# Kernel tuning notes

Measured on AMD Instinct MI355X. Metric: run time of the kernel, lower is better.

Reference implementation:

```python
import jax, jax.numpy as jnp
import numpy as np

B, T, C, WD = 8, 2048, 768, 512
TD, CD = 384, 3072   # tokens_dim=0.5*C, channels_dim=4*C
H1 = C               # default hidden of token StyleGLUs
EPS = 1e-6


def _ln(x, g, b):
    mu = jnp.mean(x, -1, keepdims=True)
    v = jnp.mean((x - mu) ** 2, -1, keepdims=True)
    return (x - mu) * jax.lax.rsqrt(v + EPS) * g + b


def _style_glu(x, w, gW, gb, sW, sb, mW, mb):
    # gate linear -> GLU -> style-modulated matmul (modulation folded into einsum)
    h = x @ gW + gb                       # [B,T,H]
    a, gt = jnp.split(h, 2, axis=-1)
    a = a * jax.nn.sigmoid(gt)            # [B,T,H/2]
    s = w @ sW + sb                       # [B,H/2] per-sample style scale
    return jnp.einsum('bth,bh,ho->bto', a, s, mW) + mb


def setup_inputs() -> dict:
    key = jax.random.key(0)
    ks = iter(jax.random.split(key, 40))
    def nrm(*s, sc=0.02):
        return jax.random.normal(next(ks), s, dtype=jnp.float32) * sc
    return dict(
        x=jax.random.normal(next(ks), (B, T, C), dtype=jnp.float32),
        w=jax.random.normal(next(ks), (B, 2, WD), dtype=jnp.float32),
        ln1_g=jnp.ones(C, jnp.float32), ln1_b=jnp.zeros(C, jnp.float32),
        ln2_g=jnp.ones(C, jnp.float32), ln2_b=jnp.zeros(C, jnp.float32),
        g1_W=nrm(C, H1), g1_b=jnp.zeros(H1, jnp.float32),
        s1_W=nrm(WD, H1 // 2), s1_b=jnp.zeros(H1 // 2, jnp.float32),
        m1_W=nrm(H1 // 2, TD, sc=0.05), m1_b=nrm(TD, sc=0.05),
        g2_W=nrm(C, H1), g2_b=jnp.zeros(H1, jnp.float32),
        s2_W=nrm(WD, H1 // 2), s2_b=jnp.zeros(H1 // 2, jnp.float32),
        m2_W=nrm(H1 // 2, TD, sc=0.05), m2_b=nrm(TD, sc=0.05),
        gs_W=nrm(C, CD), gs_b=jnp.zeros(CD, jnp.float32),
        ss_W=nrm(WD, CD // 2), ss_b=jnp.zeros(CD // 2, jnp.float32),
        ms_W=nrm(CD // 2, C, sc=0.05), ms_b=nrm(C, sc=0.05),
        r1_W=nrm(C, C), r1_b=jnp.zeros(C, jnp.float32),
        r2_W=nrm(C // 2, C), r2_b=jnp.zeros(C, jnp.float32),
    )


def reference(x, w, ln1_g, ln1_b, ln2_g, ln2_b,
              g1_W, g1_b, s1_W, s1_b, m1_W, m1_b,
              g2_W, g2_b, s2_W, s2_b, m2_W, m2_b,
              gs_W, gs_b, ss_W, ss_b, ms_W, ms_b,
              r1_W, r1_b, r2_W, r2_b):
    x = _ln(x, ln1_g, ln1_b)
    w0, w1 = w[:, 0], w[:, 1]
    # --- StyleHyperMixer token mixing (eval: dropout/droppath = identity) ---
    h1 = _style_glu(x, w0, g1_W, g1_b, s1_W, s1_b, m1_W, m1_b)  # [B,T,TD]
    h2 = _style_glu(x, w0, g2_W, g2_b, s2_W, s2_b, m2_W, m2_b)  # [B,T,TD]
    mix = jax.nn.gelu(jnp.einsum('btd,btc->bdc', h1, x), approximate=False)  # [B,TD,C]
    x = x + jnp.einsum('btd,bdc->btc', h2, mix)
    # --- style-modulated channel MLP ---
    x = x + _style_glu(_ln(x, ln2_g, ln2_b), w1, gs_W, gs_b, ss_W, ss_b, ms_W, ms_b)
    # --- GLU reduce ---
    h = x @ r1_W + r1_b
    a, gt = jnp.split(h, 2, axis=-1)
    return (a * jax.nn.sigmoid(gt)) @ r2_W + r2_b
```

## Files before the change

kernel.cpp:

```cpp
#include <hip/hip_runtime.h>
#include <hip/hip_bf16.h>
#include <math.h>

#define NB 8
#define NT 2048
#define NC 768
#define ROWS (NB*NT)

typedef __attribute__((ext_vector_type(8))) short s8v;
typedef __attribute__((ext_vector_type(4))) float f4v;

__device__ __forceinline__ unsigned short f2b(float f) {
    unsigned u = __builtin_bit_cast(unsigned, f);
    return (unsigned short)((u + 0x7FFFu + ((u >> 16) & 1u)) >> 16);
}

__device__ __forceinline__ void gll16(const ushort* g, ushort* l) {
    __builtin_amdgcn_global_load_lds(
        (const __attribute__((address_space(1))) void*)g,
        (__attribute__((address_space(3))) void*)l, 16, 0, 0);
}

template<int R>
__device__ __forceinline__ void stageL(ushort* __restrict__ L, const ushort* __restrict__ G,
                                       int ld, int r0, int k0, int lane, int w) {
    int rs = lane >> 2, c = lane & 3;
#pragma unroll
    for (int i = 0; i < R / 64; i++) {
        int ii = w + 4 * i;
        int row = ii * 16 + rs;
        int kc = (c ^ ((row >> 1) & 3)) << 3;
        gll16(G + (long)(r0 + row) * ld + k0 + kc, L + ii * 512);
    }
}

template<int R>
__device__ __forceinline__ void stage_f32(ushort* __restrict__ L, const float* __restrict__ G,
                                          int ld, int r0, int k0, int t) {
#pragma unroll
    for (int i = 0; i < R / 32; i++) {
        int e = i * 256 + t;
        int row = e >> 3, kc = (e & 7) * 4;
        float4 v = *(const float4*)(G + (long)(r0 + row) * ld + k0 + kc);
        ushort4 o;
        o.x = f2b(v.x); o.y = f2b(v.y); o.z = f2b(v.z); o.w = f2b(v.w);
        int c = (kc >> 3) ^ ((row >> 1) & 3);
        *(ushort4*)&L[row * 32 + c * 8 + (kc & 7)] = o;
    }
}

template<int TN, int EPI, bool HASBIAS, bool SPLITK>
__global__ __launch_bounds__(256) void gemm_mfma(
    const ushort* __restrict__ A, const ushort* __restrict__ Bt,
    float* __restrict__ Cf, ushort* __restrict__ Cb,
    int M, int N, int K, int lda, int ldb, int ldc,
    long sA, long sB, long sC, const float* __restrict__ bias)
{
    constexpr int WM = (TN == 128) ? 64 : 32;
    constexpr int TI = WM / 16;
    int zz = blockIdx.z;
    int z  = SPLITK ? (zz >> 2) : zz;
    int kb = SPLITK ? (zz & 3) * (K >> 2) : 0;
    int ke = SPLITK ? kb + (K >> 2) : K;
    const ushort* Az = A + (long)z * sA;
    const ushort* Bz = Bt + (long)z * sB;
    float*  Cfz = Cf ? Cf + (long)z * sC : nullptr;
    ushort* Cbz = Cb ? Cb + (long)z * sC : nullptr;

    int m0 = blockIdx.y * 128, n0 = blockIdx.x * TN;
    __shared__ alignas(16) ushort Al[4096];
    __shared__ alignas(16) ushort Bl[TN * 32];
    int t = threadIdx.x;
    int lane = t & 63, w = t >> 6;
    int wm = (TN == 128) ? (w >> 1) * 64 : w * 32;
    int wn = (TN == 128) ? (w & 1) * 64 : 0;
    int fr = lane & 15, q = lane >> 4;

    f4v acc[TI][4];
#pragma unroll
    for (int i = 0; i < TI; i++)
#pragma unroll
        for (int j = 0; j < 4; j++) acc[i][j] = (f4v)(0.0f);

    for (int k0 = kb; k0 < ke; k0 += 32) {
        stageL<128>(Al, Az, lda, m0, k0, lane, w);
        stageL<TN>(Bl, Bz, ldb, n0, k0, lane, w);
        __syncthreads();
        s8v af[TI], bf[4];
#pragma unroll
        for (int ti = 0; ti < TI; ti++) {
            int r = wm + ti * 16 + fr;
            af[ti] = *(const s8v*)&Al[r * 32 + ((q ^ ((r >> 1) & 3)) << 3)];
        }
#pragma unroll
        for (int tj = 0; tj < 4; tj++) {
            int r = wn + tj * 16 + fr;
            bf[tj] = *(const s8v*)&Bl[r * 32 + ((q ^ ((r >> 1) & 3)) << 3)];
        }
#pragma unroll
        for (int ti = 0; ti < TI; ti++)
#pragma unroll
            for (int tj = 0; tj < 4; tj++)
                acc[ti][tj] = __builtin_amdgcn_mfma_f32_16x16x32_bf16(
                    af[ti], bf[tj], acc[ti][tj], 0, 0, 0);
        __syncthreads();
    }

    int cr0 = q * 4;
#pragma unroll
    for (int ti = 0; ti < TI; ti++) {
#pragma unroll
        for (int tj = 0; tj < 4; tj++) {
            int n = n0 + wn + tj * 16 + fr;
            float bv = HASBIAS ? bias[n] : 0.0f;
#pragma unroll
            for (int r = 0; r < 4; r++) {
                int m = m0 + wm + ti * 16 + cr0 + r;
                long idx = (long)m * ldc + n;
                float v = acc[ti][tj][r] + bv;
                if (EPI == 0) {
                    Cbz[idx] = f2b(v);
                } else if (EPI == 5) {
                    Cfz[idx] = v;
                } else if (EPI == 6) {
                    __hip_atomic_fetch_add(&Cfz[idx], v, __ATOMIC_RELAXED,
                                           __HIP_MEMORY_SCOPE_AGENT);
                } else {
                    v += Cfz[idx];
                    if (EPI == 3) Cfz[idx] = v;
                    if (EPI == 4) Cbz[idx] = f2b(v);
                }
            }
        }
    }
}

template<int TN, bool HAS_S, bool AF32>
__global__ __launch_bounds__(256) void gemm_glu_mfma(
    const void* __restrict__ A,
    const ushort* __restrict__ Bt0, const ushort* __restrict__ Bt1,
    ushort* __restrict__ C0, ushort* __restrict__ C1,
    int M, int Nh, int K, int lda,
    const float* __restrict__ bias0, const float* __restrict__ bias1,
    const float* __restrict__ s0, const float* __restrict__ s1, int bofs)
{
    constexpr int WM = (TN == 128) ? 64 : 32;
    constexpr int TI = WM / 16;
    int z = blockIdx.z;
    const ushort* Bt = z ? Bt1 : Bt0;
    ushort* Cb = z ? C1 : C0;
    const float* bias = z ? bias1 : bias0;
    const float* s = z ? s1 : s0;

    int m0 = blockIdx.y * 128, n0 = blockIdx.x * TN;
    __shared__ alignas(16) ushort Al[4096];
    __shared__ alignas(16) ushort B1[TN * 32];
    __shared__ alignas(16) ushort B2[TN * 32];
    int t = threadIdx.x;
    int lane = t & 63, w = t >> 6;
    int wm = (TN == 128) ? (w >> 1) * 64 : w * 32;
    int wn = (TN == 128) ? (w & 1) * 64 : 0;
    int fr = lane & 15, q = lane >> 4;

    f4v acc1[TI][4], acc2[TI][4];
#pragma unroll
    for (int i = 0; i < TI; i++)
#pragma unroll
        for (int j = 0; j < 4; j++) { acc1[i][j] = (f4v)(0.0f); acc2[i][j] = (f4v)(0.0f); }

    for (int k0 = 0; k0 < K; k0 += 32) {
        stageL<TN>(B1, Bt, K, n0, k0, lane, w);
        stageL<TN>(B2, Bt, K, Nh + n0, k0, lane, w);
        if (AF32) stage_f32<128>(Al, (const float*)A, lda, m0, k0, t);
        else      stageL<128>(Al, (const ushort*)A, lda, m0, k0, lane, w);
        __syncthreads();
        s8v af[TI], b1f[4], b2f[4];
#pragma unroll
        for (int ti = 0; ti < TI; ti++) {
            int r = wm + ti * 16 + fr;
            af[ti] = *(const s8v*)&Al[r * 32 + ((q ^ ((r >> 1) & 3)) << 3)];
        }
#pragma unroll
        for (int tj = 0; tj < 4; tj++) {
            int r = wn + tj * 16 + fr;
            int o = r * 32 + ((q ^ ((r >> 1) & 3)) << 3);
            b1f[tj] = *(const s8v*)&B1[o];
            b2f[tj] = *(const s8v*)&B2[o];
        }
#pragma unroll
        for (int ti = 0; ti < TI; ti++)
#pragma unroll
            for (int tj = 0; tj < 4; tj++) {
                acc1[ti][tj] = __builtin_amdgcn_mfma_f32_16x16x32_bf16(af[ti], b1f[tj], acc1[ti][tj], 0, 0, 0);
                acc2[ti][tj] = __builtin_amdgcn_mfma_f32_16x16x32_bf16(af[ti], b2f[tj], acc2[ti][tj], 0, 0, 0);
            }
        __syncthreads();
    }

    int cr0 = q * 4;
#pragma unroll
    for (int ti = 0; ti < TI; ti++) {
        int bb = ((m0 + wm + ti * 16 + cr0) >> 11) + bofs;
#pragma unroll
        for (int tj = 0; tj < 4; tj++) {
            int n = n0 + wn + tj * 16 + fr;
            float bv = bias[n], bg = bias[Nh + n];
            float sv = HAS_S ? s[(long)bb * Nh + n] : 1.0f;
#pragma unroll
            for (int r = 0; r < 4; r++) {
                int m = m0 + wm + ti * 16 + cr0 + r;
                float vv = acc1[ti][tj][r] + bv;
                float gg = acc2[ti][tj][r] + bg;
                float a = vv * (1.0f / (1.0f + expf(-gg)));
                if (HAS_S) a *= sv;
                Cb[(long)m * Nh + n] = f2b(a);
            }
        }
    }
}

__global__ __launch_bounds__(256) void gelu_cast_kernel(const float* __restrict__ in,
                                                        ushort* __restrict__ out) {
    int i4 = (blockIdx.x * 256 + threadIdx.x) * 4;
    float4 v = *(const float4*)(in + i4);
    ushort4 o;
    o.x = f2b(0.5f * v.x * (1.0f + erff(v.x * 0.70710678118654752440f)));
    o.y = f2b(0.5f * v.y * (1.0f + erff(v.y * 0.70710678118654752440f)));
    o.z = f2b(0.5f * v.z * (1.0f + erff(v.z * 0.70710678118654752440f)));
    o.w = f2b(0.5f * v.w * (1.0f + erff(v.w * 0.70710678118654752440f)));
    *(ushort4*)(out + i4) = o;
}

template<bool SRC_F32>
__global__ __launch_bounds__(256) void transpose_kernel(const void* __restrict__ src,
                                                        ushort* __restrict__ dst,
                                                        int R, int C, long sS, long sD) {
    int z = blockIdx.z;
    const void* S = SRC_F32 ? (const void*)((const float*)src + (long)z * sS)
                            : (const void*)((const ushort*)src + (long)z * sS);
    ushort* D = dst + (long)z * sD;
    int r0 = blockIdx.y * 64, c0 = blockIdx.x * 64;
    __shared__ ushort T[64][68];
    int t = threadIdx.x;
#pragma unroll
    for (int p = 0; p < 4; p++) {
        int e = p * 256 + t;
        int row = e >> 4, cc = (e & 15) * 4;
        ushort4 v;
        if (SRC_F32) {
            float4 f = *(const float4*)((const float*)S + (long)(r0 + row) * C + c0 + cc);
            v.x = f2b(f.x); v.y = f2b(f.y); v.z = f2b(f.z); v.w = f2b(f.w);
        } else {
            v = *(const ushort4*)((const ushort*)S + (long)(r0 + row) * C + c0 + cc);
        }
        *(ushort4*)&T[row][cc] = v;
    }
    __syncthreads();
#pragma unroll
    for (int p = 0; p < 4; p++) {
        int e = p * 256 + t;
        int crow = e >> 4, rr = (e & 15) * 4;
        ushort4 o;
        o.x = T[rr + 0][crow]; o.y = T[rr + 1][crow];
        o.z = T[rr + 2][crow]; o.w = T[rr + 3][crow];
        *(ushort4*)&D[(long)(c0 + crow) * R + r0 + rr] = o;
    }
}

__global__ __launch_bounds__(256) void castT_kernel(const float* __restrict__ W,
                                                    ushort* __restrict__ Wt, int K, int N) {
    int k = blockIdx.x * 64 + (threadIdx.x & 63);
    int n = blockIdx.y * 4 + (threadIdx.x >> 6);
    Wt[(long)n * K + k] = f2b(W[(long)k * N + n]);
}

template<bool BF16OUT>
__global__ __launch_bounds__(256) void ln_kernel(const float* __restrict__ x,
                                                 const float* __restrict__ g,
                                                 const float* __restrict__ b,
                                                 void* __restrict__ outv) {
    int row = blockIdx.x;
    const float* xr = x + (long)row * NC;
    int t = threadIdx.x;
    float v0 = xr[t], v1 = xr[t + 256], v2 = xr[t + 512];
    float s = v0 + v1 + v2;
    float s2 = v0 * v0 + v1 * v1 + v2 * v2;
    for (int off = 32; off > 0; off >>= 1) {
        s  += __shfl_down(s, off, 64);
        s2 += __shfl_down(s2, off, 64);
    }
    __shared__ float ls[4], ls2[4];
    int wid = t >> 6, lane = t & 63;
    if (lane == 0) { ls[wid] = s; ls2[wid] = s2; }
    __syncthreads();
    if (t == 0) {
        float ts = ls[0] + ls[1] + ls[2] + ls[3];
        float ts2 = ls2[0] + ls2[1] + ls2[2] + ls2[3];
        float mu = ts * (1.0f / NC);
        float var = ts2 * (1.0f / NC) - mu * mu;
        ls[0] = mu;
        ls2[0] = 1.0f / sqrtf(var + 1e-6f);
    }
    __syncthreads();
    float mu = ls[0], r = ls2[0];
#pragma unroll
    for (int i = 0; i < 3; i++) {
        int c = t + i * 256;
        float vv = (i == 0 ? v0 : (i == 1 ? v1 : v2));
        float o = (vv - mu) * r * g[c] + b[c];
        if (BF16OUT) ((ushort*)outv)[(long)row * NC + c] = f2b(o);
        else         ((float*)outv)[(long)row * NC + c] = o;
    }
}

__global__ __launch_bounds__(256) void svec_kernel(const float* __restrict__ w,
                                                   const float* __restrict__ s1W, const float* __restrict__ s1b,
                                                   const float* __restrict__ s2W, const float* __restrict__ s2b,
                                                   const float* __restrict__ ssW, const float* __restrict__ ssb,
                                                   float* __restrict__ sout) {
    int gid = blockIdx.x * 256 + threadIdx.x;
    int bb = gid / 2304;
    int r  = gid % 2304;
    const float* w0 = w + (long)bb * 1024;
    const float* w1 = w0 + 512;
    float acc = 0.f;
    if (r < 384) {
        for (int k = 0; k < 512; k++) acc += w0[k] * s1W[k * 384 + r];
        sout[bb * 384 + r] = acc + s1b[r];
    } else if (r < 768) {
        int c = r - 384;
        for (int k = 0; k < 512; k++) acc += w0[k] * s2W[k * 384 + c];
        sout[3072 + bb * 384 + c] = acc + s2b[c];
    } else {
        int c = r - 768;
        for (int k = 0; k < 512; k++) acc += w1[k] * ssW[k * 1536 + c];
        sout[6144 + bb * 1536 + c] = acc + ssb[c];
    }
}

extern "C" void kernel_launch(void* const* d_in, const int* in_sizes, int n_in,
                              void* d_out, int out_size, void* d_ws, size_t ws_size,
                              hipStream_t stream) {
    const float* x     = (const float*)d_in[0];
    const float* w     = (const float*)d_in[1];
    const float* ln1_g = (const float*)d_in[2];
    const float* ln1_b = (const float*)d_in[3];
    const float* ln2_g = (const float*)d_in[4];
    const float* ln2_b = (const float*)d_in[5];
    const float* g1_W  = (const float*)d_in[6];
    const float* g1_b  = (const float*)d_in[7];
    const float* s1_W  = (const float*)d_in[8];
    const float* s1_b  = (const float*)d_in[9];
    const float* m1_W  = (const float*)d_in[10];
    const float* m1_b  = (const float*)d_in[11];
    const float* g2_W  = (const float*)d_in[12];
    const float* g2_b  = (const float*)d_in[13];
    const float* s2_W  = (const float*)d_in[14];
    const float* s2_b  = (const float*)d_in[15];
    const float* m2_W  = (const float*)d_in[16];
    const float* m2_b  = (const float*)d_in[17];
    const float* gs_W  = (const float*)d_in[18];
    const float* gs_b  = (const float*)d_in[19];
    const float* ss_W  = (const float*)d_in[20];
    const float* ss_b  = (const float*)d_in[21];
    const float* ms_W  = (const float*)d_in[22];
    const float* ms_b  = (const float*)d_in[23];
    const float* r1_W  = (const float*)d_in[24];
    const float* r1_b  = (const float*)d_in[25];
    const float* r2_W  = (const float*)d_in[26];
    const float* r2_b  = (const float*)d_in[27];
    float* out = (float*)d_out;
    char* ws = (char*)d_ws;
    char* ob = (char*)d_out;

    float*  XLN = (float*)ws;
    ushort* A1b = (ushort*)(ws + 50331648);
    ushort* g1t = (ushort*)(ws + 62914560);
    ushort* g2t = g1t + 589824;
    ushort* m1t = g2t + 589824;
    ushort* m2t = m1t + 147456;
    ushort* gst = m2t + 147456;
    ushort* mst = gst + 2359296;
    ushort* r1t = mst + 1179648;
    ushort* r2t = r1t + 589824;
    float*  SV  = (float*)(ws + 74711040);
    ushort* H1T = A1b;
    ushort* ASq = A1b;
    ushort* ARq = A1b;

    ushort* XLNT  = (ushort*)(ob + 25165824);
    ushort* A2q   = (ushort*)(ob + 12582912);
    ushort* H2q   = (ushort*)ob;
    ushort* H1q   = (ushort*)(ob + 12582912);
    float*  MIXTf = (float*)(ob + 12582912);
    ushort* MIXTb = (ushort*)(ob + 25165824);
    ushort* X2LNq = (ushort*)(ob + 25165824);
    ushort* X3q   = (ushort*)ob;

    castT_kernel<<<dim3(12, 192), 256, 0, stream>>>(g1_W, g1t, 768, 768);
    castT_kernel<<<dim3(12, 192), 256, 0, stream>>>(g2_W, g2t, 768, 768);
    castT_kernel<<<dim3(6,  96),  256, 0, stream>>>(m1_W, m1t, 384, 384);
    castT_kernel<<<dim3(6,  96),  256, 0, stream>>>(m2_W, m2t, 384, 384);
    castT_kernel<<<dim3(12, 768), 256, 0, stream>>>(gs_W, gst, 768, 3072);
    castT_kernel<<<dim3(24, 192), 256, 0, stream>>>(ms_W, mst, 1536, 768);
    castT_kernel<<<dim3(12, 192), 256, 0, stream>>>(r1_W, r1t, 768, 768);
    castT_kernel<<<dim3(6,  192), 256, 0, stream>>>(r2_W, r2t, 384, 768);
    svec_kernel<<<72, 256, 0, stream>>>(w, s1_W, s1_b, s2_W, s2_b, ss_W, ss_b, SV);
    ln_kernel<false><<<ROWS, 256, 0, stream>>>(x, ln1_g, ln1_b, XLN);
    transpose_kernel<true><<<dim3(12, 32, NB), 256, 0, stream>>>(
        XLN, XLNT, 2048, 768, (long)2048 * 768, (long)768 * 2048);

    gemm_glu_mfma<128, true, true><<<dim3(3, 128, 2), 256, 0, stream>>>(
        XLN, g1t, g2t, A1b, A2q, ROWS, 384, 768, 768, g1_b, g2_b, SV, SV + 3072, 0);
    gemm_mfma<64, 0, true, false><<<dim3(6, 128), 256, 0, stream>>>(
        A2q, m2t, nullptr, H2q, ROWS, 384, 384, 384, 384, 384, 0, 0, 0, m2_b);
    gemm_mfma<64, 0, true, false><<<dim3(6, 128), 256, 0, stream>>>(
        A1b, m1t, nullptr, H1q, ROWS, 384, 384, 384, 384, 384, 0, 0, 0, m1_b);
    transpose_kernel<false><<<dim3(6, 32, NB), 256, 0, stream>>>(
        H1q, H1T, 2048, 384, (long)2048 * 384, (long)384 * 2048);
    hipMemsetAsync(MIXTf, 0, (size_t)NB * 768 * 384 * 4, stream);
    gemm_mfma<128, 6, false, true><<<dim3(3, 6, NB * 4), 256, 0, stream>>>(
        XLNT, H1T, MIXTf, nullptr, 768, 384, 2048, 2048, 2048, 384,
        (long)768 * 2048, (long)384 * 2048, (long)768 * 384, nullptr);
    gelu_cast_kernel<<<2304, 256, 0, stream>>>(MIXTf, MIXTb);
    gemm_mfma<128, 3, false, false><<<dim3(6, 16, NB), 256, 0, stream>>>(
        H2q, MIXTb, XLN, nullptr, 2048, 768, 384, 384, 384, 768,
        (long)2048 * 384, (long)768 * 384, (long)2048 * 768, nullptr);
    ln_kernel<true><<<ROWS, 256, 0, stream>>>(XLN, ln2_g, ln2_b, X2LNq);
    for (int ch = 0; ch < 4; ch++) {
        ushort* X2c = X2LNq + (long)ch * 4096 * 768;
        float*  XLNc = XLN + (long)ch * 4096 * 768;
        ushort* X3c = X3q + (long)ch * 4096 * 768;
        gemm_glu_mfma<64, true, false><<<dim3(24, 32), 256, 0, stream>>>(
            X2c, gst, gst, ASq, ASq, 4096, 1536, 768, 768, gs_b, gs_b,
            SV + 6144, SV + 6144, ch * 2);
        gemm_mfma<64, 4, true, false><<<dim3(12, 32), 256, 0, stream>>>(
            ASq, mst, XLNc, X3c, 4096, 768, 1536, 1536, 1536, 768, 0, 0, 0, ms_b);
    }
    gemm_glu_mfma<64, false, false><<<dim3(6, 128), 256, 0, stream>>>(
        X3q, r1t, r1t, ARq, ARq, ROWS, 384, 768, 768, r1_b, r1_b, nullptr, nullptr, 0);
    gemm_mfma<128, 5, true, false><<<dim3(6, 128), 256, 0, stream>>>(
        ARq, r2t, out, nullptr, ROWS, 768, 384, 384, 384, 768, 0, 0, 0, r2_b);
}
```

Before: 859.1 us.

## Merge weight-cast launches into one prep kernel and emit bf16 from first LN

Eight weight cast/transpose launches and the style-vector kernel are merged into a single prep kernel, which cuts launch overhead. The first layernorm now writes both fp32 and bf16 outputs, so the first GLU GEMM can stage its A tiles with direct global-to-LDS loads instead of converting fp32 per k-step. The sigmoid switches to the fast __expf, and the transpose launch is reordered after the GLU GEMM. In exchange the LN pass writes an extra bf16 copy, and __expf gives slightly lower precision.

Result: faster. 822.0 us (-4.3%).

```diff
diff --git a/kernel.cpp b/kernel.cpp
--- a/kernel.cpp
+++ b/kernel.cpp
@@ -31,21 +31,6 @@
         int row = ii * 16 + rs;
         int kc = (c ^ ((row >> 1) & 3)) << 3;
         gll16(G + (long)(r0 + row) * ld + k0 + kc, L + ii * 512);
-    }
-}
-
-template<int R>
-__device__ __forceinline__ void stage_f32(ushort* __restrict__ L, const float* __restrict__ G,
-                                          int ld, int r0, int k0, int t) {
-#pragma unroll
-    for (int i = 0; i < R / 32; i++) {
-        int e = i * 256 + t;
-        int row = e >> 3, kc = (e & 7) * 4;
-        float4 v = *(const float4*)(G + (long)(r0 + row) * ld + k0 + kc);
-        ushort4 o;
-        o.x = f2b(v.x); o.y = f2b(v.y); o.z = f2b(v.z); o.w = f2b(v.w);
-        int c = (kc >> 3) ^ ((row >> 1) & 3);
-        *(ushort4*)&L[row * 32 + c * 8 + (kc & 7)] = o;
     }
 }
 
@@ -135,9 +120,9 @@
     }
 }
 
-template<int TN, bool HAS_S, bool AF32>
+template<int TN, bool HAS_S>
 __global__ __launch_bounds__(256) void gemm_glu_mfma(
-    const void* __restrict__ A,
+    const ushort* __restrict__ A,
     const ushort* __restrict__ Bt0, const ushort* __restrict__ Bt1,
     ushort* __restrict__ C0, ushort* __restrict__ C1,
     int M, int Nh, int K, int lda,
@@ -171,8 +156,7 @@
     for (int k0 = 0; k0 < K; k0 += 32) {
         stageL<TN>(B1, Bt, K, n0, k0, lane, w);
         stageL<TN>(B2, Bt, K, Nh + n0, k0, lane, w);
-        if (AF32) stage_f32<128>(Al, (const float*)A, lda, m0, k0, t);
-        else      stageL<128>(Al, (const ushort*)A, lda, m0, k0, lane, w);
+        stageL<128>(Al, A, lda, m0, k0, lane, w);
         __syncthreads();
         s8v af[TI], b1f[4], b2f[4];
 #pragma unroll
@@ -211,7 +195,7 @@
                 int m = m0 + wm + ti * 16 + cr0 + r;
                 float vv = acc1[ti][tj][r] + bv;
                 float gg = acc2[ti][tj][r] + bg;
-                float a = vv * (1.0f / (1.0f + expf(-gg)));
+                float a = vv * (1.0f / (1.0f + __expf(-gg)));
                 if (HAS_S) a *= sv;
                 Cb[(long)m * Nh + n] = f2b(a);
             }
@@ -267,18 +251,64 @@
     }
 }
 
-__global__ __launch_bounds__(256) void castT_kernel(const float* __restrict__ W,
-                                                    ushort* __restrict__ Wt, int K, int N) {
-    int k = blockIdx.x * 64 + (threadIdx.x & 63);
-    int n = blockIdx.y * 4 + (threadIdx.x >> 6);
-    Wt[(long)n * K + k] = f2b(W[(long)k * N + n]);
-}
-
-template<bool BF16OUT>
+__global__ __launch_bounds__(256) void prep_kernel(
+    const float* __restrict__ g1_W, ushort* __restrict__ g1t,
+    const float* __restrict__ g2_W, ushort* __restrict__ g2t,
+    const float* __restrict__ m1_W, ushort* __restrict__ m1t,
+    const float* __restrict__ m2_W, ushort* __restrict__ m2t,
+    const float* __restrict__ gs_W, ushort* __restrict__ gst,
+    const float* __restrict__ ms_W, ushort* __restrict__ mst,
+    const float* __restrict__ r1_W, ushort* __restrict__ r1t,
+    const float* __restrict__ r2_W, ushort* __restrict__ r2t,
+    const float* __restrict__ w,
+    const float* __restrict__ s1W, const float* __restrict__ s1b,
+    const float* __restrict__ s2W, const float* __restrict__ s2b,
+    const float* __restrict__ ssW, const float* __restrict__ ssb,
+    float* __restrict__ sout)
+{
+    int b = blockIdx.x, t = threadIdx.x;
+    if (b < 23040) {
+        const float* W; ushort* Wt; int K, N, lo;
+        if      (b < 2304)  { W = g1_W; Wt = g1t; K = 768;  N = 768;  lo = 0; }
+        else if (b < 4608)  { W = g2_W; Wt = g2t; K = 768;  N = 768;  lo = 2304; }
+        else if (b < 5184)  { W = m1_W; Wt = m1t; K = 384;  N = 384;  lo = 4608; }
+        else if (b < 5760)  { W = m2_W; Wt = m2t; K = 384;  N = 384;  lo = 5184; }
+        else if (b < 14976) { W = gs_W; Wt = gst; K = 768;  N = 3072; lo = 5760; }
+        else if (b < 19584) { W = ms_W; Wt = mst; K = 1536; N = 768;  lo = 14976; }
+        else if (b < 21888) { W = r1_W; Wt = r1t; K = 768;  N = 768;  lo = 19584; }
+        else                { W = r2_W; Wt = r2t; K = 384;  N = 768;  lo = 21888; }
+        int local = b - lo, bx = K >> 6;
+        int byi = local / bx, bxi = local - byi * bx;
+        int k = bxi * 64 + (t & 63), n = byi * 4 + (t >> 6);
+        Wt[(long)n * K + k] = f2b(W[(long)k * N + n]);
+    } else {
+        int gid = (b - 23040) * 256 + t;
+        int bb = gid / 2304;
+        int r  = gid % 2304;
+        const float* w0 = w + (long)bb * 1024;
+        const float* w1 = w0 + 512;
+        float acc = 0.f;
+        if (r < 384) {
+            for (int k = 0; k < 512; k++) acc += w0[k] * s1W[k * 384 + r];
+            sout[bb * 384 + r] = acc + s1b[r];
+        } else if (r < 768) {
+            int c = r - 384;
+            for (int k = 0; k < 512; k++) acc += w0[k] * s2W[k * 384 + c];
+            sout[3072 + bb * 384 + c] = acc + s2b[c];
+        } else {
+            int c = r - 768;
+            for (int k = 0; k < 512; k++) acc += w1[k] * ssW[k * 1536 + c];
+            sout[6144 + bb * 1536 + c] = acc + ssb[c];
+        }
+    }
+}
+
+template<int MODE>
 __global__ __launch_bounds__(256) void ln_kernel(const float* __restrict__ x,
                                                  const float* __restrict__ g,
                                                  const float* __restrict__ b,
-                                                 void* __restrict__ outv) {
+                                                 float* __restrict__ outf,
+                                                 ushort* __restrict__ outb) {
     int row = blockIdx.x;
     const float* xr = x + (long)row * NC;
     int t = threadIdx.x;
@@ -308,33 +338,8 @@
         int c = t + i * 256;
         float vv = (i == 0 ? v0 : (i == 1 ? v1 : v2));
         float o = (vv - mu) * r * g[c] + b[c];
-        if (BF16OUT) ((ushort*)outv)[(long)row * NC + c] = f2b(o);
-        else         ((float*)outv)[(long)row * NC + c] = o;
-    }
-}
-
-__global__ __launch_bounds__(256) void svec_kernel(const float* __restrict__ w,
-                                                   const float* __restrict__ s1W, const float* __restrict__ s1b,
-                                                   const float* __restrict__ s2W, const float* __restrict__ s2b,
-                                                   const float* __restrict__ ssW, const float* __restrict__ ssb,
-                                                   float* __restrict__ sout) {
-    int gid = blockIdx.x * 256 + threadIdx.x;
-    int bb = gid / 2304;
-    int r  = gid % 2304;
-    const float* w0 = w + (long)bb * 1024;
-    const float* w1 = w0 + 512;
-    float acc = 0.f;
-    if (r < 384) {
-        for (int k = 0; k < 512; k++) acc += w0[k] * s1W[k * 384 + r];
-        sout[bb * 384 + r] = acc + s1b[r];
-    } else if (r < 768) {
-        int c = r - 384;
-        for (int k = 0; k < 512; k++) acc += w0[k] * s2W[k * 384 + c];
-        sout[3072 + bb * 384 + c] = acc + s2b[c];
-    } else {
-        int c = r - 768;
-        for (int k = 0; k < 512; k++) acc += w1[k] * ssW[k * 1536 + c];
-        sout[6144 + bb * 1536 + c] = acc + ssb[c];
+        if (MODE == 2) outf[(long)row * NC + c] = o;
+        outb[(long)row * NC + c] = f2b(o);
     }
 }
 
@@ -388,6 +393,7 @@
     ushort* ASq = A1b;
     ushort* ARq = A1b;
 
+    ushort* XLNb  = (ushort*)(ob + 25165824);
     ushort* XLNT  = (ushort*)(ob + 25165824);
     ushort* A2q   = (ushort*)(ob + 12582912);
     ushort* H2q   = (ushort*)ob;
@@ -397,21 +403,15 @@
     ushort* X2LNq = (ushort*)(ob + 25165824);
     ushort* X3q   = (ushort*)ob;
 
-    castT_kernel<<<dim3(12, 192), 256, 0, stream>>>(g1_W, g1t, 768, 768);
-    castT_kernel<<<dim3(12, 192), 256, 0, stream>>>(g2_W, g2t, 768, 768);
-    castT_kernel<<<dim3(6,  96),  256, 0, stream>>>(m1_W, m1t, 384, 384);
-    castT_kernel<<<dim3(6,  96),  256, 0, stream>>>(m2_W, m2t, 384, 384);
-    castT_kernel<<<dim3(12, 768), 256, 0, stream>>>(gs_W, gst, 768, 3072);
-    castT_kernel<<<dim3(24, 192), 256, 0, stream>>>(ms_W, mst, 1536, 768);
-    castT_kernel<<<dim3(12, 192), 256, 0, stream>>>(r1_W, r1t, 768, 768);
-    castT_kernel<<<dim3(6,  192), 256, 0, stream>>>(r2_W, r2t, 384, 768);
-    svec_kernel<<<72, 256, 0, stream>>>(w, s1_W, s1_b, s2_W, s2_b, ss_W, ss_b, SV);
-    ln_kernel<false><<<ROWS, 256, 0, stream>>>(x, ln1_g, ln1_b, XLN);
+    prep_kernel<<<23112, 256, 0, stream>>>(
+        g1_W, g1t, g2_W, g2t, m1_W, m1t, m2_W, m2t, gs_W, gst, ms_W, mst,
+        r1_W, r1t, r2_W, r2t, w, s1_W, s1_b, s2_W, s2_b, ss_W, ss_b, SV);
+    ln_kernel<2><<<ROWS, 256, 0, stream>>>(x, ln1_g, ln1_b, XLN, XLNb);
+
+    gemm_glu_mfma<128, true><<<dim3(3, 128, 2), 256, 0, stream>>>(
+        XLNb, g1t, g2t, A1b, A2q, ROWS, 384, 768, 768, g1_b, g2_b, SV, SV + 3072, 0);
     transpose_kernel<true><<<dim3(12, 32, NB), 256, 0, stream>>>(
         XLN, XLNT, 2048, 768, (long)2048 * 768, (long)768 * 2048);
-
-    gemm_glu_mfma<128, true, true><<<dim3(3, 128, 2), 256, 0, stream>>>(
-        XLN, g1t, g2t, A1b, A2q, ROWS, 384, 768, 768, g1_b, g2_b, SV, SV + 3072, 0);
     gemm_mfma<64, 0, true, false><<<dim3(6, 128), 256, 0, stream>>>(
         A2q, m2t, nullptr, H2q, ROWS, 384, 384, 384, 384, 384, 0, 0, 0, m2_b);
     gemm_mfma<64, 0, true, false><<<dim3(6, 128), 256, 0, stream>>>(
@@ -426,18 +426,18 @@
     gemm_mfma<128, 3, false, false><<<dim3(6, 16, NB), 256, 0, stream>>>(
         H2q, MIXTb, XLN, nullptr, 2048, 768, 384, 384, 384, 768,
         (long)2048 * 384, (long)768 * 384, (long)2048 * 768, nullptr);
-    ln_kernel<true><<<ROWS, 256, 0, stream>>>(XLN, ln2_g, ln2_b, X2LNq);
+    ln_kernel<1><<<ROWS, 256, 0, stream>>>(XLN, ln2_g, ln2_b, nullptr, X2LNq);
     for (int ch = 0; ch < 4; ch++) {
         ushort* X2c = X2LNq + (long)ch * 4096 * 768;
         float*  XLNc = XLN + (long)ch * 4096 * 768;
         ushort* X3c = X3q + (long)ch * 4096 * 768;
-        gemm_glu_mfma<64, true, false><<<dim3(24, 32), 256, 0, stream>>>(
+        gemm_glu_mfma<64, true><<<dim3(24, 32), 256, 0, stream>>>(
             X2c, gst, gst, ASq, ASq, 4096, 1536, 768, 768, gs_b, gs_b,
             SV + 6144, SV + 6144, ch * 2);
         gemm_mfma<64, 4, true, false><<<dim3(12, 32), 256, 0, stream>>>(
             ASq, mst, XLNc, X3c, 4096, 768, 1536, 1536, 1536, 768, 0, 0, 0, ms_b);
     }
-    gemm_glu_mfma<64, false, false><<<dim3(6, 128), 256, 0, stream>>>(
+    gemm_glu_mfma<64, false><<<dim3(6, 128), 256, 0, stream>>>(
         X3q, r1t, r1t, ARq, ARq, ROWS, 384, 768, 768, r1_b, r1_b, nullptr, nullptr, 0);
     gemm_mfma<128, 5, true, false><<<dim3(6, 128), 256, 0, stream>>>(
         ARq, r2t, out, nullptr, ROWS, 768, 384, 384, 384, 768, 0, 0, 0, r2_b);
```
